# Optimization experiments

Hardware: AMD Instinct MI355X
Metric: run time of the kernel (lower is better)

Reference implementation:

```python
import jax, jax.numpy as jnp
import numpy as np

B, S, D, H = 32, 1024, 192, 8
DH = D // H  # 24


def setup_inputs() -> dict:
    key = jax.random.key(0)
    ks = jax.random.split(key, 8)
    s_in = 1.0 / np.sqrt(D)
    return {
        "x": jax.random.normal(ks[0], (B, S, D), dtype=jnp.float32),
        "mask": jax.random.randint(ks[1], (B, S), 0, 2).astype(bool),
        "Wq": jax.random.normal(ks[2], (H, D, DH), dtype=jnp.float32) * s_in,
        "bq": jnp.zeros((H, DH), dtype=jnp.float32),
        "Wk": jax.random.normal(ks[3], (H, D, DH), dtype=jnp.float32) * s_in,
        "bk": jnp.zeros((H, DH), dtype=jnp.float32),
        "Wv": jax.random.normal(ks[4], (H, D, DH), dtype=jnp.float32) * s_in,
        "bv": jnp.zeros((H, DH), dtype=jnp.float32),
        "Wo": jax.random.normal(ks[5], (D, D), dtype=jnp.float32) * s_in,
        "bo": jnp.zeros((D,), dtype=jnp.float32),
    }


def reference(x, mask, Wq, bq, Wk, bk, Wv, bv, Wo, bo):
    # Batched per-head projections: [B,S,D] x [H,D,DH] -> [B,H,S,DH]
    q = jnp.einsum("bsd,hde->bhse", x, Wq) + bq[None, :, None, :]
    k = jnp.einsum("bsd,hde->bhse", x, Wk) + bk[None, :, None, :]
    v = jnp.einsum("bsd,hde->bhse", x, Wv) + bv[None, :, None, :]
    scale = 1.0 / np.sqrt(DH).astype(np.float32)
    scores = jnp.einsum("bhse,bhte->bhst", q, k) * scale  # [B,H,S,S]
    # mask [B,S] broadcast over heads and query positions (masked_fill with -1e9)
    scores = jnp.where(mask[:, None, None, :], scores, -1e9)
    weights = jax.nn.softmax(scores, axis=-1)
    out = jnp.einsum("bhst,bhte->bhse", weights, v)  # [B,H,S,DH]
    # concat heads along last dim -> [B,S,D]
    out = out.transpose(0, 2, 1, 3).reshape(B, S, D)
    return out @ Wo + bo
```

## Files before the change

### kernel.cpp

```cpp
#include <hip/hip_runtime.h>

typedef __attribute__((ext_vector_type(8))) short short8;
typedef __attribute__((ext_vector_type(4))) float f32x4;
typedef __attribute__((ext_vector_type(16))) float f32x16;
typedef __attribute__((ext_vector_type(2))) unsigned uint2v;
typedef __attribute__((ext_vector_type(4))) unsigned uint4v;

#define MFMA16(a,b,c) __builtin_amdgcn_mfma_f32_16x16x32_bf16((a),(b),(c),0,0,0)
#define MFMA32(a,b,c) __builtin_amdgcn_mfma_f32_32x32x16_bf16((a),(b),(c),0,0,0)

#define BB 32
#define SS 1024
#define DD 192
#define HH 8
#define DHP 32

#define SCALE_Q 0.294468266742895f

__device__ __forceinline__ short nb(float f) {
    __bf16 h = (__bf16)f;
    return __builtin_bit_cast(short, h);
}
__device__ __forceinline__ float bf2f(short s) {
    union { unsigned u; float f; } v; v.u = ((unsigned)(unsigned short)s) << 16;
    return v.f;
}
__device__ __forceinline__ unsigned pk2(float a, float b) {
    unsigned short lo = __builtin_bit_cast(unsigned short, (__bf16)a);
    unsigned short hi = __builtin_bit_cast(unsigned short, (__bf16)b);
    return (unsigned)lo | ((unsigned)hi << 16);
}

#define NBLK_PREP 720
#define NBLK_XPREP 512
__global__ __launch_bounds__(256) void setup_kernel(
    const float* __restrict__ Wq, const float* __restrict__ Wk, const float* __restrict__ Wv,
    const float* __restrict__ Wo, const float* __restrict__ x, const void* __restrict__ mask_raw,
    short* __restrict__ WqF, short* __restrict__ WkF, short* __restrict__ WvF,
    short* __restrict__ WoFh, short* __restrict__ xF,
    float* __restrict__ maskf, int* __restrict__ fwd, int* __restrict__ cnt)
{
    __shared__ short lds[64][200];
    int bid = blockIdx.x;
    int t = threadIdx.x;

    if (bid < NBLK_PREP) {
        int idx = bid * 256 + t;
        const int NWX = 3 * HH * DHP * DD;
        const int NWO = DD * DD;
        if (idx < NWX) {
            int mat = idx / (HH * DHP * DD);
            int jj  = idx % (HH * DHP * DD);
            int h   = jj / (DHP * DD);
            int rem = jj % (DHP * DD);
            int e   = rem / DD;
            int d   = rem % DD;
            const float* W = (mat == 0) ? Wq : (mat == 1) ? Wk : Wv;
            short* WF      = (mat == 0) ? WqF : (mat == 1) ? WkF : WvF;
            float val = (e < 24) ? W[(h * DD + d) * 24 + e] : 0.f;
            int nt = e & 1, cc = e >> 1;
            int kk = d >> 5, g = (d >> 3) & 3, ee = d & 7;
            WF[(size_t)((((h*2+nt)*6 + kk)*64) + g*16 + cc)*8 + ee] = nb(val);
        } else if (idx < NWX + NWO) {
            int j = idx - NWX;
            int n = j / DD, k = j % DD;
            int nn = n >> 4, cc = n & 15;
            int kk = k >> 5, g = (k >> 3) & 3, ee = k & 7;
            WoFh[(size_t)(((nn*6 + kk)*64) + g*16 + cc)*8 + ee] = nb(Wo[k * DD + n]);
        }
    } else if (bid < NBLK_PREP + NBLK_XPREP) {
        int xb = bid - NBLK_PREP;
        int r0 = xb * 64;
        #pragma unroll
        for (int i = 0; i < 12; i++) {
            int idx = i * 256 + t;
            int row = idx / 48;
            int colf = (idx % 48) * 4;
            float4 f = *(const float4*)(x + ((size_t)(r0 + row)) * DD + colf);
            lds[row][colf + 0] = nb(f.x);
            lds[row][colf + 1] = nb(f.y);
            lds[row][colf + 2] = nb(f.z);
            lds[row][colf + 3] = nb(f.w);
        }
        __syncthreads();
        int w = t >> 6, lane = t & 63, c = lane & 15, g = lane >> 4;
        short* outb = xF + (size_t)(xb * 4 + w) * 6 * 512;
        #pragma unroll
        for (int kk = 0; kk < 6; kk++) {
            short8 o = *(const short8*)&lds[w * 16 + c][kk * 32 + g * 8];
            *(short8*)(outb + kk * 512 + (size_t)lane * 8) = o;
        }
    } else {
        int b = bid - NBLK_PREP - NBLK_XPREP;
        int lane = t & 63, wv = t >> 6;
        int* wsu = (int*)&lds[0][0];

        const unsigned* mw = (const unsigned*)mask_raw;
        bool all01 = true, allf = true;
        #pragma unroll
        for (int i = 0; i < 16; i++) {
            unsigned w = mw[i];
            all01 = all01 && (w <= 1u);
            allf  = allf  && (w == 0u || w == 0x3F800000u);
        }
        int s0 = t * 4;
        bool m[4];
        #pragma unroll
        for (int j = 0; j < 4; j++) {
            int idx = b * SS + s0 + j;
            bool mm;
            if (all01)      mm = (mw[idx] != 0u);
            else if (allf)  mm = (((const float*)mask_raw)[idx] != 0.f);
            else            mm = (((const unsigned char*)mask_raw)[idx] != 0);
            m[j] = mm;
            maskf[idx] = mm ? 1.f : 0.f;
        }
        int cnt4 = (int)m[0] + (int)m[1] + (int)m[2] + (int)m[3];
        int pref = cnt4;
        #pragma unroll
        for (int d = 1; d < 64; d <<= 1) {
            int o = __shfl_up(pref, d, 64);
            if (lane >= d) pref += o;
        }
        int waveExcl = pref - cnt4;
        if (lane == 63) wsu[wv] = pref;
        __syncthreads();
        int waveOff = 0, totalU = 0;
        #pragma unroll
        for (int i = 0; i < 4; i++) {
            int v = wsu[i];
            if (i < wv) waveOff += v;
            totalU += v;
        }
        int pu = waveOff + waveExcl;
        #pragma unroll
        for (int j = 0; j < 4; j++) {
            int s = s0 + j;
            if (m[j]) { fwd[b * SS + pu] = s; pu++; }
            else      { fwd[b * SS + totalU + (s - pu)] = s; }
        }
        if (t == 0) cnt[b] = totalU;
    }
}

__global__ __launch_bounds__(256) void proj_kernel(
    const short* __restrict__ xF,
    const float* __restrict__ bq, const float* __restrict__ bk, const float* __restrict__ bv,
    const short* __restrict__ WqF, const short* __restrict__ WkF, const short* __restrict__ WvF,
    const float* __restrict__ maskf,
    short* __restrict__ Q, short* __restrict__ Kc, short* __restrict__ Vc)
{
    int tid = threadIdx.x;
    int lane = tid & 63, w = tid >> 6;
    int c = lane & 15, g = lane >> 4;
    int r0 = blockIdx.x * 64 + w * 16;
    int h = blockIdx.y;

    int b_ = r0 >> 10;
    int s0 = (r0 & 1023) + g * 4;
    int bh = b_ * HH + h;

    short8 a[6];
    const short* xfb = xF + (size_t)(r0 >> 4) * 6 * 512 + (size_t)lane * 8;
    #pragma unroll
    for (int kk = 0; kk < 6; kk++)
        a[kk] = *(const short8*)(xfb + kk * 512);

    float mrow[4];
    #pragma unroll
    for (int r = 0; r < 4; r++) mrow[r] = maskf[b_ * SS + s0 + r];

    #pragma unroll
    for (int mat = 0; mat < 3; mat++) {
        const short* WF   = (mat==0)?WqF:(mat==1)?WkF:WvF;
        const float* bias = (mat==0)?bq:(mat==1)?bk:bv;

        f32x4 acc0 = {0.f,0.f,0.f,0.f};
        f32x4 acc1 = {0.f,0.f,0.f,0.f};
        const short* Wp0 = WF + (size_t)((h*2+0)*6) * 512 + lane * 8;
        const short* Wp1 = WF + (size_t)((h*2+1)*6) * 512 + lane * 8;
        #pragma unroll
        for (int kk = 0; kk < 6; kk++) {
            short8 b0 = *(const short8*)(Wp0 + kk * 512);
            short8 b1 = *(const short8*)(Wp1 + kk * 512);
            acc0 = MFMA16(a[kk], b0, acc0);
            acc1 = MFMA16(a[kk], b1, acc1);
        }
        float bv0 = 0.f, bv1 = 0.f;
        if (2*c < 24) {
            float2 bb = *(const float2*)(bias + h * 24 + 2 * c);
            bv0 = bb.x; bv1 = bb.y;
        }

        if (mat == 0) {
            #pragma unroll
            for (int r = 0; r < 4; r++) {
                float v0 = (acc0[r] + bv0) * SCALE_Q;
                float v1 = (c == 15) ? 1.0f : (acc1[r] + bv1) * SCALE_Q;
                *(unsigned*)(Q + ((size_t)bh * SS + s0 + r) * DHP + 2*c) = pk2(v0, v1);
            }
        } else if (mat == 1) {
            #pragma unroll
            for (int r = 0; r < 4; r++) {
                float v0 = acc0[r] + bv0;
                float v1 = (c == 15) ? ((mrow[r] != 0.f) ? 0.f : -1e30f)
                                     : (acc1[r] + bv1);
                *(unsigned*)(Kc + ((size_t)bh * SS + s0 + r) * DHP + 2*c) = pk2(v0, v1);
            }
        } else {
            #pragma unroll
            for (int r = 0; r < 4; r++) {
                float v0 = (c == 12) ? 1.0f : (acc0[r] + bv0);
                float v1 = acc1[r] + bv1;
                *(unsigned*)(Vc + ((size_t)bh * SS + s0 + r) * DHP + 2*c) = pk2(v0, v1);
            }
        }
    }
}

__global__ __launch_bounds__(256) void kvprep_kernel(
    const short* __restrict__ Kc, const short* __restrict__ Vc,
    const int* __restrict__ fwd, const int* __restrict__ cnt,
    short* __restrict__ KF, short* __restrict__ VF)
{
    int bh = blockIdx.x, c4 = blockIdx.y;
    int b = bh >> 3;
    int nt32 = ((cnt[b] + 31) >> 5) << 5;
    int row0 = c4 * 128;
    if (row0 >= nt32) return;

    __shared__ short lds[128][40];
    int t = threadIdx.x;
    int srow[2];

    #pragma unroll
    for (int p = 0; p < 2; p++) {
        int j = p * 64 + (t >> 2);
        int part = t & 3;
        int s = fwd[b * SS + row0 + j];
        srow[p] = s;
        *(short8*)&lds[j][part * 8] =
            *(const short8*)(Kc + ((size_t)bh * SS + s) * DHP + part * 8);
    }
    __syncthreads();

    int tile_l = t >> 6, L = t & 63, l31 = L & 31, hi = L >> 5;
    short* kf0 = KF + (size_t)bh * SS * DHP + (size_t)(row0 / 32 + tile_l) * 1024;
    #pragma unroll
    for (int i = 0; i < 2; i++) {
        short8 o = *(const short8*)&lds[tile_l * 32 + l31][i * 16 + hi * 8];
        *(short8*)(kf0 + i * 512 + (size_t)L * 8) = o;
    }
    __syncthreads();

    #pragma unroll
    for (int p = 0; p < 2; p++) {
        int j = p * 64 + (t >> 2);
        int part = t & 3;
        *(short8*)&lds[j][part * 8] =
            *(const short8*)(Vc + ((size_t)bh * SS + srow[p]) * DHP + part * 8);
    }
    __syncthreads();

    short* vf0 = VF + (size_t)bh * SS * DHP + (size_t)(row0 / 32 + tile_l) * 1024;
    #pragma unroll
    for (int i = 0; i < 2; i++) {
        short8 o;
        #pragma unroll
        for (int j2 = 0; j2 < 8; j2++)
            o[j2] = lds[tile_l * 32 + i * 16 + hi * 8 + j2][l31];
        *(short8*)(vf0 + i * 512 + (size_t)L * 8) = o;
    }
}

__device__ __forceinline__ void fproc(const f32x16& S, f32x16& acc,
                                      short8 v0, short8 v1)
{
    float p[16];
    #pragma unroll
    for (int r = 0; r < 16; r++) p[r] = __builtin_amdgcn_exp2f(S[r]);

    unsigned c01 = pk2(p[0],  p[1]);
    unsigned c23 = pk2(p[2],  p[3]);
    unsigned c45 = pk2(p[4],  p[5]);
    unsigned c67 = pk2(p[6],  p[7]);
    unsigned c89 = pk2(p[8],  p[9]);
    unsigned cab = pk2(p[10], p[11]);
    unsigned ccd = pk2(p[12], p[13]);
    unsigned cef = pk2(p[14], p[15]);

    uint2v s0 = __builtin_amdgcn_permlane32_swap(c01, c45, false, false);
    uint2v s1 = __builtin_amdgcn_permlane32_swap(c23, c67, false, false);
    uint2v s2 = __builtin_amdgcn_permlane32_swap(c89, ccd, false, false);
    uint2v s3 = __builtin_amdgcn_permlane32_swap(cab, cef, false, false);

    uint4v w0v = { s0.x, s1.x, s0.y, s1.y };
    uint4v w1v = { s2.x, s3.x, s2.y, s3.y };
    short8 pa0 = __builtin_bit_cast(short8, w0v);
    short8 pa1 = __builtin_bit_cast(short8, w1v);

    acc = MFMA32(pa0, v0, acc);
    acc = MFMA32(pa1, v1, acc);
}

__global__ __launch_bounds__(256, 2) void flash_kernel(
    const short* __restrict__ Q, const short* __restrict__ KF, const short* __restrict__ VF,
    const int* __restrict__ cnt, short* __restrict__ Af)
{
    __shared__ float llds[4][4][32];

    int idx = blockIdx.x;
    int bh = idx & 255;
    int qb = idx >> 8;
    int b = bh >> 3, h = bh & 7;

    int tid = threadIdx.x;
    int lane = tid & 63, w = tid >> 6;
    int l31 = lane & 31;
    int hi = lane >> 5;

    int nt = (cnt[b] + 31) >> 5;

    int qr0 = qb * 512 + w * 32;

    short8 qf[4][2];
    #pragma unroll
    for (int cc = 0; cc < 4; cc++) {
        const short* Qp = Q + ((size_t)bh * SS + qr0 + cc * 128 + l31) * DHP + hi * 8;
        qf[cc][0] = *(const short8*)Qp;
        qf[cc][1] = *(const short8*)(Qp + 16);
    }

    const short* Kp = KF + (size_t)bh * SS * DHP + (size_t)lane * 8;
    const short* Vp = VF + (size_t)bh * SS * DHP + (size_t)lane * 8;

    f32x16 acc[4], Z16;
    #pragma unroll
    for (int r = 0; r < 16; r++) {
        acc[0][r] = 0.f; acc[1][r] = 0.f; acc[2][r] = 0.f; acc[3][r] = 0.f;
        Z16[r] = 0.f;
    }

    short8 k0 = *(const short8*)(Kp);
    short8 k1 = *(const short8*)(Kp + 512);
    short8 v0 = *(const short8*)(Vp);
    short8 v1 = *(const short8*)(Vp + 512);

    for (int kt = 0; kt < nt; kt++) {
        Kp += 1024;
        Vp += 1024;
        short8 nk0 = *(const short8*)(Kp);
        short8 nk1 = *(const short8*)(Kp + 512);
        short8 nv0 = *(const short8*)(Vp);
        short8 nv1 = *(const short8*)(Vp + 512);

        #pragma unroll
        for (int cc = 0; cc < 4; cc++) {
            f32x16 S = MFMA32(k0, qf[cc][0], Z16);
            S = MFMA32(k1, qf[cc][1], S);
            fproc(S, acc[cc], v0, v1);
        }

        k0 = nk0; k1 = nk1; v0 = nv0; v1 = nv1;
    }

    if (l31 == 24) {
        #pragma unroll
        for (int cc = 0; cc < 4; cc++) {
            #pragma unroll
            for (int r = 0; r < 16; r++) {
                int row = (r & 3) + 8 * (r >> 2) + 4 * hi;
                llds[w][cc][row] = __builtin_amdgcn_rcpf(acc[cc][r]);
            }
        }
    }
    __builtin_amdgcn_wave_barrier();

    if (l31 < 24) {
        int d = h * 24 + l31;
        size_t fcol = (size_t)((d >> 5) * 4 + ((d >> 3) & 3)) * 128 + (d & 7);
        #pragma unroll
        for (int cc = 0; cc < 4; cc++) {
            int grp = (b * SS + qr0 + cc * 128) >> 4;
            short* op = Af + (size_t)grp * 3072 + fcol;
            #pragma unroll
            for (int r = 0; r < 16; r++) {
                int row = (r & 3) + 8 * (r >> 2) + 4 * hi;
                size_t off = (size_t)(r >> 3) * 3072 + (size_t)(row & 15) * 8;
                op[off] = nb(acc[cc][r] * llds[w][cc][row]);
            }
        }
    }
}

__global__ __launch_bounds__(256) void final_kernel(
    const short* __restrict__ Af,
    const short* __restrict__ WoFh,
    const float* __restrict__ bo, float* __restrict__ out)
{
    int tid = threadIdx.x;
    int lane = tid & 63, w = tid >> 6;
    int c = lane & 15, g = lane >> 4;
    int r0 = blockIdx.x * 64 + w * 16;
    int n0 = blockIdx.y * 3;

    short8 a[6];
    #pragma unroll
    for (int kk = 0; kk < 6; kk++)
        a[kk] = *(const short8*)(Af + ((size_t)(r0 >> 4) * 24 + kk*4 + g) * 128 + c * 8);

    f32x4 acc[3];
    #pragma unroll
    for (int n = 0; n < 3; n++) acc[n] = (f32x4){0.f,0.f,0.f,0.f};

    #pragma unroll
    for (int kk = 0; kk < 6; kk++) {
        #pragma unroll
        for (int n = 0; n < 3; n++) {
            short8 bh = *(const short8*)(WoFh + (size_t)((n0+n)*6 + kk) * 512 + lane * 8);
            acc[n] = MFMA16(a[kk], bh, acc[n]);
        }
    }

    #pragma unroll
    for (int n = 0; n < 3; n++) {
        int col = (n0+n)*16 + c;
        float bv = bo[col];
        #pragma unroll
        for (int r = 0; r < 4; r++) {
            out[(size_t)(r0 + g*4 + r) * DD + col] = acc[n][r] + bv;
        }
    }
}

extern "C" void kernel_launch(void* const* d_in, const int* in_sizes, int n_in,
                              void* d_out, int out_size, void* d_ws, size_t ws_size,
                              hipStream_t stream)
{
    const float* x    = (const float*)d_in[0];
    const void*  mask = d_in[1];
    const float* Wq   = (const float*)d_in[2];
    const float* bq   = (const float*)d_in[3];
    const float* Wk   = (const float*)d_in[4];
    const float* bk   = (const float*)d_in[5];
    const float* Wv   = (const float*)d_in[6];
    const float* bv   = (const float*)d_in[7];
    const float* Wo   = (const float*)d_in[8];
    const float* bo   = (const float*)d_in[9];
    float* out = (float*)d_out;

    char* ws = (char*)d_ws;
    size_t off = 0;
    float* maskf = (float*)(ws + off); off += (size_t)BB*SS*4;
    short* Q     = (short*)(ws + off); off += (size_t)BB*HH*SS*DHP*2;
    short* Kc    = (short*)(ws + off); off += (size_t)BB*HH*SS*DHP*2;
    short* Vc    = (short*)(ws + off); off += (size_t)BB*HH*SS*DHP*2;
    short* KF    = (short*)(ws + off); off += (size_t)BB*HH*SS*DHP*2;
    short* VF    = (short*)(ws + off); off += (size_t)BB*HH*SS*DHP*2;
    short* xF    = (short*)(ws + off); off += (size_t)BB*SS*DD*2;
    short* WqF   = (short*)(ws + off); off += (size_t)HH*DHP*DD*2;
    short* WkF   = (short*)(ws + off); off += (size_t)HH*DHP*DD*2;
    short* WvF   = (short*)(ws + off); off += (size_t)HH*DHP*DD*2;
    short* WoFh  = (short*)(ws + off); off += (size_t)DD*DD*2;
    int*   fwd   = (int*)  (ws + off); off += (size_t)BB*SS*4;
    int*   cnt   = (int*)  (ws + off); off += 256;

    short* Af = Kc;

    setup_kernel<<<dim3(NBLK_PREP + NBLK_XPREP + BB), dim3(256), 0, stream>>>(
        Wq, Wk, Wv, Wo, x, mask, WqF, WkF, WvF, WoFh, xF, maskf, fwd, cnt);
    proj_kernel<<<dim3(512, 8), dim3(256), 0, stream>>>(
        xF, bq, bk, bv, WqF, WkF, WvF, maskf, Q, Kc, Vc);
    kvprep_kernel<<<dim3(256, 8), dim3(256), 0, stream>>>(
        Kc, Vc, fwd, cnt, KF, VF);
    flash_kernel<<<dim3(512), dim3(256), 0, stream>>>(
        Q, KF, VF, cnt, Af);
    final_kernel<<<dim3(512, 4), dim3(256), 0, stream>>>(
        Af, WoFh, bo, out);
}
```

Measured before the change: 91.94 us.

## Fuse K/V projection with compaction gather into a single projection kernel

Merges the projection and KV-compaction kernels into one launch. Q blocks still project from the pre-packed x. K/V blocks gather the unmasked rows of x directly via the forward index, project them, and write K/V straight into the MFMA-friendly compacted layout through LDS. This removes the intermediate Kc/Vc buffers and one kernel launch, and skips projecting K/V for masked rows. In exchange it re-reads fp32 x with a scattered row gather, adds several block barriers per head, and needs a larger LDS footprint.

Measured after the change: 89.13 us. 1.03x faster.

```diff
diff --git a/kernel.cpp b/kernel.cpp
--- a/kernel.cpp
+++ b/kernel.cpp
@@ -20,10 +20,6 @@
 __device__ __forceinline__ short nb(float f) {
     __bf16 h = (__bf16)f;
     return __builtin_bit_cast(short, h);
-}
-__device__ __forceinline__ float bf2f(short s) {
-    union { unsigned u; float f; } v; v.u = ((unsigned)(unsigned short)s) << 16;
-    return v.f;
 }
 __device__ __forceinline__ unsigned pk2(float a, float b) {
     unsigned short lo = __builtin_bit_cast(unsigned short, (__bf16)a);
@@ -143,133 +139,159 @@
     }
 }
 
-__global__ __launch_bounds__(256) void proj_kernel(
-    const short* __restrict__ xF,
+__global__ __launch_bounds__(256) void proj2_kernel(
+    const float* __restrict__ x, const short* __restrict__ xF,
     const float* __restrict__ bq, const float* __restrict__ bk, const float* __restrict__ bv,
     const short* __restrict__ WqF, const short* __restrict__ WkF, const short* __restrict__ WvF,
-    const float* __restrict__ maskf,
-    short* __restrict__ Q, short* __restrict__ Kc, short* __restrict__ Vc)
-{
-    int tid = threadIdx.x;
-    int lane = tid & 63, w = tid >> 6;
+    const float* __restrict__ maskf, const int* __restrict__ fwd, const int* __restrict__ cnt,
+    short* __restrict__ Q, short* __restrict__ KF, short* __restrict__ VF)
+{
+    __shared__ short lds[64][200];
+    __shared__ int   srows[64];
+    __shared__ short klds[64][40];
+
+    int bid = blockIdx.x;
+    int t = threadIdx.x;
+    int lane = t & 63, w = t >> 6;
     int c = lane & 15, g = lane >> 4;
-    int r0 = blockIdx.x * 64 + w * 16;
-    int h = blockIdx.y;
-
-    int b_ = r0 >> 10;
-    int s0 = (r0 & 1023) + g * 4;
-    int bh = b_ * HH + h;
-
-    short8 a[6];
-    const short* xfb = xF + (size_t)(r0 >> 4) * 6 * 512 + (size_t)lane * 8;
-    #pragma unroll
-    for (int kk = 0; kk < 6; kk++)
-        a[kk] = *(const short8*)(xfb + kk * 512);
-
-    float mrow[4];
-    #pragma unroll
-    for (int r = 0; r < 4; r++) mrow[r] = maskf[b_ * SS + s0 + r];
-
-    #pragma unroll
-    for (int mat = 0; mat < 3; mat++) {
-        const short* WF   = (mat==0)?WqF:(mat==1)?WkF:WvF;
-        const float* bias = (mat==0)?bq:(mat==1)?bk:bv;
-
-        f32x4 acc0 = {0.f,0.f,0.f,0.f};
-        f32x4 acc1 = {0.f,0.f,0.f,0.f};
-        const short* Wp0 = WF + (size_t)((h*2+0)*6) * 512 + lane * 8;
-        const short* Wp1 = WF + (size_t)((h*2+1)*6) * 512 + lane * 8;
-        #pragma unroll
-        for (int kk = 0; kk < 6; kk++) {
-            short8 b0 = *(const short8*)(Wp0 + kk * 512);
-            short8 b1 = *(const short8*)(Wp1 + kk * 512);
-            acc0 = MFMA16(a[kk], b0, acc0);
-            acc1 = MFMA16(a[kk], b1, acc1);
-        }
-        float bv0 = 0.f, bv1 = 0.f;
-        if (2*c < 24) {
-            float2 bb = *(const float2*)(bias + h * 24 + 2 * c);
-            bv0 = bb.x; bv1 = bb.y;
-        }
-
-        if (mat == 0) {
+
+    if (bid < 2048) {
+        int rb = bid & 511, hp = bid >> 9;
+        int r0 = rb * 64 + w * 16;
+        int b_ = r0 >> 10;
+        int s0 = (r0 & 1023) + g * 4;
+
+        short8 a[6];
+        const short* xfb = xF + (size_t)(r0 >> 4) * 6 * 512 + (size_t)lane * 8;
+        #pragma unroll
+        for (int kk = 0; kk < 6; kk++)
+            a[kk] = *(const short8*)(xfb + kk * 512);
+
+        #pragma unroll
+        for (int hh = 0; hh < 2; hh++) {
+            int h = hp * 2 + hh;
+            int bh = b_ * HH + h;
+            f32x4 acc0 = {0.f,0.f,0.f,0.f};
+            f32x4 acc1 = {0.f,0.f,0.f,0.f};
+            const short* Wp0 = WqF + (size_t)((h*2+0)*6) * 512 + lane * 8;
+            const short* Wp1 = WqF + (size_t)((h*2+1)*6) * 512 + lane * 8;
+            #pragma unroll
+            for (int kk = 0; kk < 6; kk++) {
+                short8 b0 = *(const short8*)(Wp0 + kk * 512);
+                short8 b1 = *(const short8*)(Wp1 + kk * 512);
+                acc0 = MFMA16(a[kk], b0, acc0);
+                acc1 = MFMA16(a[kk], b1, acc1);
+            }
+            float bv0 = 0.f, bv1 = 0.f;
+            if (2*c < 24) {
+                float2 bb = *(const float2*)(bq + h * 24 + 2 * c);
+                bv0 = bb.x; bv1 = bb.y;
+            }
             #pragma unroll
             for (int r = 0; r < 4; r++) {
                 float v0 = (acc0[r] + bv0) * SCALE_Q;
                 float v1 = (c == 15) ? 1.0f : (acc1[r] + bv1) * SCALE_Q;
                 *(unsigned*)(Q + ((size_t)bh * SS + s0 + r) * DHP + 2*c) = pk2(v0, v1);
             }
-        } else if (mat == 1) {
-            #pragma unroll
-            for (int r = 0; r < 4; r++) {
-                float v0 = acc0[r] + bv0;
-                float v1 = (c == 15) ? ((mrow[r] != 0.f) ? 0.f : -1e30f)
-                                     : (acc1[r] + bv1);
-                *(unsigned*)(Kc + ((size_t)bh * SS + s0 + r) * DHP + 2*c) = pk2(v0, v1);
-            }
-        } else {
-            #pragma unroll
-            for (int r = 0; r < 4; r++) {
-                float v0 = (c == 12) ? 1.0f : (acc0[r] + bv0);
-                float v1 = acc1[r] + bv1;
-                *(unsigned*)(Vc + ((size_t)bh * SS + s0 + r) * DHP + 2*c) = pk2(v0, v1);
-            }
-        }
-    }
-}
-
-__global__ __launch_bounds__(256) void kvprep_kernel(
-    const short* __restrict__ Kc, const short* __restrict__ Vc,
-    const int* __restrict__ fwd, const int* __restrict__ cnt,
-    short* __restrict__ KF, short* __restrict__ VF)
-{
-    int bh = blockIdx.x, c4 = blockIdx.y;
-    int b = bh >> 3;
+        }
+        return;
+    }
+
+    int kb = bid - 2048;
+    int chunk = kb & 15, hp = (kb >> 4) & 3, b = kb >> 6;
+    int row0 = chunk * 64;
     int nt32 = ((cnt[b] + 31) >> 5) << 5;
-    int row0 = c4 * 128;
     if (row0 >= nt32) return;
 
-    __shared__ short lds[128][40];
-    int t = threadIdx.x;
-    int srow[2];
-
-    #pragma unroll
-    for (int p = 0; p < 2; p++) {
-        int j = p * 64 + (t >> 2);
-        int part = t & 3;
+    {
+        int j = t >> 2, part = t & 3;
         int s = fwd[b * SS + row0 + j];
-        srow[p] = s;
-        *(short8*)&lds[j][part * 8] =
-            *(const short8*)(Kc + ((size_t)bh * SS + s) * DHP + part * 8);
+        if (part == 0) srows[j] = s;
+        const float* xr = x + ((size_t)(b * SS + s)) * DD + part * 48;
+        #pragma unroll
+        for (int i = 0; i < 12; i++) {
+            float4 f = *(const float4*)(xr + i * 4);
+            int col = part * 48 + i * 4;
+            *(unsigned*)&lds[j][col]     = pk2(f.x, f.y);
+            *(unsigned*)&lds[j][col + 2] = pk2(f.z, f.w);
+        }
     }
     __syncthreads();
 
-    int tile_l = t >> 6, L = t & 63, l31 = L & 31, hi = L >> 5;
-    short* kf0 = KF + (size_t)bh * SS * DHP + (size_t)(row0 / 32 + tile_l) * 1024;
-    #pragma unroll
-    for (int i = 0; i < 2; i++) {
-        short8 o = *(const short8*)&lds[tile_l * 32 + l31][i * 16 + hi * 8];
-        *(short8*)(kf0 + i * 512 + (size_t)L * 8) = o;
-    }
-    __syncthreads();
-
-    #pragma unroll
-    for (int p = 0; p < 2; p++) {
-        int j = p * 64 + (t >> 2);
-        int part = t & 3;
-        *(short8*)&lds[j][part * 8] =
-            *(const short8*)(Vc + ((size_t)bh * SS + srow[p]) * DHP + part * 8);
-    }
-    __syncthreads();
-
-    short* vf0 = VF + (size_t)bh * SS * DHP + (size_t)(row0 / 32 + tile_l) * 1024;
-    #pragma unroll
-    for (int i = 0; i < 2; i++) {
-        short8 o;
-        #pragma unroll
-        for (int j2 = 0; j2 < 8; j2++)
-            o[j2] = lds[tile_l * 32 + i * 16 + hi * 8 + j2][l31];
-        *(short8*)(vf0 + i * 512 + (size_t)L * 8) = o;
+    short8 a[6];
+    #pragma unroll
+    for (int kk = 0; kk < 6; kk++)
+        a[kk] = *(const short8*)&lds[w * 16 + c][kk * 32 + g * 8];
+
+    float mrow[4];
+    #pragma unroll
+    for (int r = 0; r < 4; r++)
+        mrow[r] = maskf[b * SS + srows[w * 16 + g * 4 + r]];
+
+    int l31 = lane & 31, hi = lane >> 5;
+
+    #pragma unroll
+    for (int hh = 0; hh < 2; hh++) {
+        int h = hp * 2 + hh;
+        int bh = b * HH + h;
+
+        f32x4 aK0 = {0.f,0.f,0.f,0.f}, aK1 = {0.f,0.f,0.f,0.f};
+        f32x4 aV0 = {0.f,0.f,0.f,0.f}, aV1 = {0.f,0.f,0.f,0.f};
+        const short* Kp0 = WkF + (size_t)((h*2+0)*6) * 512 + lane * 8;
+        const short* Kp1 = WkF + (size_t)((h*2+1)*6) * 512 + lane * 8;
+        const short* Vp0 = WvF + (size_t)((h*2+0)*6) * 512 + lane * 8;
+        const short* Vp1 = WvF + (size_t)((h*2+1)*6) * 512 + lane * 8;
+        #pragma unroll
+        for (int kk = 0; kk < 6; kk++) {
+            aK0 = MFMA16(a[kk], *(const short8*)(Kp0 + kk * 512), aK0);
+            aK1 = MFMA16(a[kk], *(const short8*)(Kp1 + kk * 512), aK1);
+            aV0 = MFMA16(a[kk], *(const short8*)(Vp0 + kk * 512), aV0);
+            aV1 = MFMA16(a[kk], *(const short8*)(Vp1 + kk * 512), aV1);
+        }
+        float bk0 = 0.f, bk1 = 0.f, bvv0 = 0.f, bvv1 = 0.f;
+        if (2*c < 24) {
+            float2 kb2 = *(const float2*)(bk + h * 24 + 2 * c);
+            float2 vb2 = *(const float2*)(bv + h * 24 + 2 * c);
+            bk0 = kb2.x; bk1 = kb2.y; bvv0 = vb2.x; bvv1 = vb2.y;
+        }
+
+        __syncthreads();
+        #pragma unroll
+        for (int r = 0; r < 4; r++) {
+            float v0 = aK0[r] + bk0;
+            float v1 = (c == 15) ? ((mrow[r] != 0.f) ? 0.f : -1e30f) : (aK1[r] + bk1);
+            *(unsigned*)&klds[w * 16 + g * 4 + r][2 * c] = pk2(v0, v1);
+        }
+        __syncthreads();
+        if (t < 128) {
+            int tt = (t >> 6) & 1, L = t & 63, l3 = L & 31, h2 = L >> 5;
+            short* kf0 = KF + (size_t)bh * SS * DHP + (size_t)(row0 / 32 + tt) * 1024;
+            #pragma unroll
+            for (int i = 0; i < 2; i++) {
+                short8 o = *(const short8*)&klds[tt * 32 + l3][i * 16 + h2 * 8];
+                *(short8*)(kf0 + i * 512 + (size_t)L * 8) = o;
+            }
+        }
+        __syncthreads();
+        #pragma unroll
+        for (int r = 0; r < 4; r++) {
+            float v0 = (c == 12) ? 1.0f : (aV0[r] + bvv0);
+            float v1 = aV1[r] + bvv1;
+            *(unsigned*)&klds[w * 16 + g * 4 + r][2 * c] = pk2(v0, v1);
+        }
+        __syncthreads();
+        if (t < 128) {
+            int tt = (t >> 6) & 1, L = t & 63, l3 = L & 31, h2 = L >> 5;
+            short* vf0 = VF + (size_t)bh * SS * DHP + (size_t)(row0 / 32 + tt) * 1024;
+            #pragma unroll
+            for (int i = 0; i < 2; i++) {
+                short8 o;
+                #pragma unroll
+                for (int j2 = 0; j2 < 8; j2++)
+                    o[j2] = klds[tt * 32 + i * 16 + h2 * 8 + j2][l3];
+                *(short8*)(vf0 + i * 512 + (size_t)L * 8) = o;
+            }
+        }
     }
 }
 
@@ -453,10 +475,9 @@
     size_t off = 0;
     float* maskf = (float*)(ws + off); off += (size_t)BB*SS*4;
     short* Q     = (short*)(ws + off); off += (size_t)BB*HH*SS*DHP*2;
-    short* Kc    = (short*)(ws + off); off += (size_t)BB*HH*SS*DHP*2;
-    short* Vc    = (short*)(ws + off); off += (size_t)BB*HH*SS*DHP*2;
     short* KF    = (short*)(ws + off); off += (size_t)BB*HH*SS*DHP*2;
     short* VF    = (short*)(ws + off); off += (size_t)BB*HH*SS*DHP*2;
+    short* Af    = (short*)(ws + off); off += (size_t)BB*SS*DD*2;
     short* xF    = (short*)(ws + off); off += (size_t)BB*SS*DD*2;
     short* WqF   = (short*)(ws + off); off += (size_t)HH*DHP*DD*2;
     short* WkF   = (short*)(ws + off); off += (size_t)HH*DHP*DD*2;
@@ -465,14 +486,10 @@
     int*   fwd   = (int*)  (ws + off); off += (size_t)BB*SS*4;
     int*   cnt   = (int*)  (ws + off); off += 256;
 
-    short* Af = Kc;
-
     setup_kernel<<<dim3(NBLK_PREP + NBLK_XPREP + BB), dim3(256), 0, stream>>>(
         Wq, Wk, Wv, Wo, x, mask, WqF, WkF, WvF, WoFh, xF, maskf, fwd, cnt);
-    proj_kernel<<<dim3(512, 8), dim3(256), 0, stream>>>(
-        xF, bq, bk, bv, WqF, WkF, WvF, maskf, Q, Kc, Vc);
-    kvprep_kernel<<<dim3(256, 8), dim3(256), 0, stream>>>(
-        Kc, Vc, fwd, cnt, KF, VF);
+    proj2_kernel<<<dim3(4096), dim3(256), 0, stream>>>(
+        x, xF, bq, bk, bv, WqF, WkF, WvF, maskf, fwd, cnt, Q, KF, VF);
     flash_kernel<<<dim3(512), dim3(256), 0, stream>>>(
         Q, KF, VF, cnt, Af);
     final_kernel<<<dim3(512, 4), dim3(256), 0, stream>>>(
```
